# Optimization experiments

Measured on AMD Instinct MI355X. Metric: run time of the kernel, lower is better.

Reference implementation:

```python
import jax, jax.numpy as jnp
import numpy as np

N = 100000
E = 1600000
F_IN = 1024
H = 128
OUT = 32
EPS = 1e-07
TOTAL_COUNT = 10000.0
BN_EPS = 1e-5


def setup_inputs() -> dict:
    key = jax.random.key(0)
    ks = jax.random.split(key, 16)
    x = jax.random.uniform(ks[0], (N, F_IN), dtype=jnp.float32)
    edge_index = jax.random.randint(ks[1], (2, E), 0, N, dtype=jnp.int64)
    def nrm(k, shape, scale=0.05):
        return jax.random.normal(k, shape, dtype=jnp.float32) * scale
    return {
        "x": x,
        "edge_index": edge_index,
        "W0": nrm(ks[2], (F_IN, H)),
        "a_s0": nrm(ks[3], (H,)),
        "a_d0": nrm(ks[4], (H,)),
        "g0": jnp.ones((H,), jnp.float32),
        "b0": jnp.zeros((H,), jnp.float32),
        "W1": nrm(ks[5], (H, H)),
        "a_s1": nrm(ks[6], (H,)),
        "a_d1": nrm(ks[7], (H,)),
        "g1": jnp.ones((H,), jnp.float32),
        "b1": jnp.zeros((H,), jnp.float32),
        "locW": nrm(ks[8], (H, OUT)),
        "locb": jnp.zeros((OUT,), jnp.float32),
        "stdW": nrm(ks[9], (H, OUT)),
        "stdb": jnp.zeros((OUT,), jnp.float32),
    }


def gat_conv(h, src, dst, W, a_s, a_d, n_nodes):
    # PyG GATConv, heads=1, concat=False, no self-loops, no bias
    h2 = h @ W                       # [N, H]
    alpha_s = h2 @ a_s               # [N]
    alpha_d = h2 @ a_d               # [N]
    e = jax.nn.leaky_relu(alpha_s[src] + alpha_d[dst], 0.2)  # [E]
    m = jax.ops.segment_max(e, dst, num_segments=n_nodes)    # [N]
    w = jnp.exp(e - m[dst])                                  # [E]
    denom = jax.ops.segment_sum(w, dst, num_segments=n_nodes)
    msg = w[:, None] * h2[src]                               # [E, H]
    out = jax.ops.segment_sum(msg, dst, num_segments=n_nodes)
    return out / (denom[:, None] + 1e-16)


def batchnorm(h, gamma, beta):
    mu = jnp.mean(h, axis=0)
    var = jnp.mean(jnp.square(h - mu), axis=0)
    return gamma * (h - mu) * jax.lax.rsqrt(var + BN_EPS) + beta


def reference(x, edge_index, W0, a_s0, a_d0, g0, b0, W1, a_s1, a_d1, g1, b1,
              locW, locb, stdW, stdb):
    src, dst = edge_index[0], edge_index[1]
    n = x.shape[0]
    l = jnp.sum(x, axis=1, keepdims=True)                 # library size
    ptr = jnp.log1p(x * (TOTAL_COUNT / l))                # normalize
    for (W, a_s, a_d, g, b) in ((W0, a_s0, a_d0, g0, b0), (W1, a_s1, a_d1, g1, b1)):
        ptr = gat_conv(ptr, src, dst, W, a_s, a_d, n)
        ptr = batchnorm(ptr, g, b)
        ptr = jax.nn.leaky_relu(ptr, 0.2)
        # dropout = identity (eval mode)
    loc = ptr @ locW + locb
    std = jax.nn.softplus(ptr @ stdW + stdb) + EPS
    return (loc, std, l)
```

## Files before the change

### kernel.cpp

```cpp
#include <hip/hip_runtime.h>

#define NN 100000
#define EE 1600000
#define FIN 1024
#define HH 128
#define OUTD 32
#define TOTC 10000.0f

typedef float f32x4 __attribute__((ext_vector_type(4)));
typedef short bf16x8 __attribute__((ext_vector_type(8)));
typedef short short4v __attribute__((ext_vector_type(4)));

static __device__ __forceinline__ short f2bf(float f) {
    unsigned u = __float_as_uint(f);
    unsigned r = (u + 0x7fffu + ((u >> 16) & 1u)) >> 16;
    return (short)r;
}

__global__ void zero_k(int* __restrict__ p, int n) {
    int i = blockIdx.x * 256 + threadIdx.x;
    if (i < n) p[i] = 0;
}

__global__ __launch_bounds__(256) void rowsum_k(const float* __restrict__ x,
                                                float* __restrict__ lout) {
    int row = blockIdx.x;
    int tid = threadIdx.x;
    const float4* px = (const float4*)(x + (long)row * FIN);
    float4 v = px[tid];
    float s = v.x + v.y + v.z + v.w;
#pragma unroll
    for (int o = 32; o; o >>= 1) s += __shfl_xor(s, o);
    __shared__ float ws[4];
    if ((tid & 63) == 0) ws[tid >> 6] = s;
    __syncthreads();
    if (tid == 0) lout[row] = ws[0] + ws[1] + ws[2] + ws[3];
}

__global__ void convW0_k(const float* __restrict__ W, short* __restrict__ BT) {
    int idx = blockIdx.x * 256 + threadIdx.x;
    int n = idx >> 10, k = idx & 1023;
    BT[idx] = f2bf(W[(long)k * HH + n]);
}
__global__ void convW1_k(const float* __restrict__ W, short* __restrict__ BT) {
    int idx = blockIdx.x * 256 + threadIdx.x;
    int n = idx >> 7, k = idx & 127;
    BT[idx] = f2bf(W[k * HH + n]);
}
__global__ void convWH_k(const float* __restrict__ locW, const float* __restrict__ stdW,
                         short* __restrict__ BT) {
    int idx = blockIdx.x * 256 + threadIdx.x;
    int n = idx >> 7, k = idx & 127;
    float v = (n < 32) ? locW[k * OUTD + n] : ((n < 64) ? stdW[k * OUTD + (n - 32)] : 0.0f);
    BT[idx] = f2bf(v);
}

__global__ void hist_k(const int* __restrict__ dst, int* __restrict__ cnt, int e) {
    int i = blockIdx.x * 256 + threadIdx.x;
    if (i < e) atomicAdd(cnt + dst[i], 1);
}

__global__ __launch_bounds__(256) void scanA_k(const int* __restrict__ cnt,
                                               int* __restrict__ out,
                                               int* __restrict__ partials, int n) {
    __shared__ int sc[256];
    int tid = threadIdx.x;
    int base = blockIdx.x * 1024 + tid * 4;
    int c[4];
#pragma unroll
    for (int u = 0; u < 4; u++) c[u] = (base + u < n) ? cnt[base + u] : 0;
    int s = c[0] + c[1] + c[2] + c[3];
    sc[tid] = s;
    __syncthreads();
    for (int of = 1; of < 256; of <<= 1) {
        int v = (tid >= of) ? sc[tid - of] : 0;
        __syncthreads();
        sc[tid] += v;
        __syncthreads();
    }
    int e = sc[tid] - s;
#pragma unroll
    for (int u = 0; u < 4; u++) {
        if (base + u < n) out[base + u] = e;
        e += c[u];
    }
    if (tid == 255) partials[blockIdx.x] = sc[255];
}

__global__ __launch_bounds__(128) void scanB_k(int* __restrict__ partials, int nblk) {
    __shared__ int sc[128];
    int tid = threadIdx.x;
    int v = (tid < nblk) ? partials[tid] : 0;
    sc[tid] = v;
    __syncthreads();
    for (int of = 1; of < 128; of <<= 1) {
        int t2 = (tid >= of) ? sc[tid - of] : 0;
        __syncthreads();
        sc[tid] += t2;
        __syncthreads();
    }
    if (tid < nblk) partials[tid] = sc[tid] - v;
}

__global__ void scanC_k(int* __restrict__ rp, const int* __restrict__ offs, int n, int total) {
    int i = blockIdx.x * 256 + threadIdx.x;
    if (i < n) rp[i] += offs[i >> 10];
    if (i == 0) rp[n] = total;
}

__global__ void fill_k(const int* __restrict__ src, const int* __restrict__ dst,
                       const int* __restrict__ rp, int* __restrict__ cur,
                       int* __restrict__ cs, int e) {
    int i = blockIdx.x * 256 + threadIdx.x;
    if (i < e) {
        int d = dst[i];
        int p = atomicAdd(cur + d, 1);
        cs[rp[d] + p] = src[i];
    }
}

#define LDP 88

template <int ASRC, int EPI>
__global__ __launch_bounds__(256) void gemm_k(
    const void* __restrict__ Ap, const float* __restrict__ lvec,
    const short* __restrict__ BT, float* __restrict__ C,
    const float* __restrict__ bias_loc, const float* __restrict__ bias_std,
    float* __restrict__ out_loc, float* __restrict__ out_std, int M, int K) {
    __shared__ short sA[128 * LDP];
    __shared__ short sB[128 * LDP];
    __shared__ float sScale[128];
    const int tid = threadIdx.x;
    const int row0 = blockIdx.x * 128;
    if (ASRC == 0) {
        if (tid < 128) {
            int g = row0 + tid;
            sScale[tid] = (g < M) ? (TOTC / lvec[g]) : 0.0f;
        }
    }
    __syncthreads();

    const int lane = tid & 63;
    const int wv = tid >> 6;
    const int wm = (wv & 1) * 64, wn = (wv >> 1) * 64;
    const int lm = lane & 15, q = lane >> 4;

    f32x4 acc[4][4];
#pragma unroll
    for (int i = 0; i < 4; i++)
#pragma unroll
        for (int j = 0; j < 4; j++) acc[i][j] = {0.f, 0.f, 0.f, 0.f};

    const int r = tid >> 1;
    const int cb = (tid & 1) * 32;
    const int gr = row0 + r;

    for (int kk = 0; kk < K; kk += 64) {
        if (ASRC == 0) {
            const float* X = (const float*)Ap;
            const float s = sScale[r];
            if (gr < M) {
                const float4* px = (const float4*)(X + (long)gr * K + kk + cb);
#pragma unroll
                for (int u = 0; u < 8; ++u) {
                    float4 v = px[u];
                    short4v o;
                    o.x = f2bf(__logf(fmaf(v.x, s, 1.0f)));
                    o.y = f2bf(__logf(fmaf(v.y, s, 1.0f)));
                    o.z = f2bf(__logf(fmaf(v.z, s, 1.0f)));
                    o.w = f2bf(__logf(fmaf(v.w, s, 1.0f)));
                    *(short4v*)&sA[r * LDP + cb + u * 4] = o;
                }
            } else {
                short4v z;
                z.x = z.y = z.z = z.w = 0;
#pragma unroll
                for (int u = 0; u < 8; ++u) *(short4v*)&sA[r * LDP + cb + u * 4] = z;
            }
        } else {
            const short* A = (const short*)Ap;
            if (gr < M) {
                const short4v* pa = (const short4v*)(A + (long)gr * K + kk + cb);
#pragma unroll
                for (int u = 0; u < 8; ++u) *(short4v*)&sA[r * LDP + cb + u * 4] = pa[u];
            } else {
                short4v z;
                z.x = z.y = z.z = z.w = 0;
#pragma unroll
                for (int u = 0; u < 8; ++u) *(short4v*)&sA[r * LDP + cb + u * 4] = z;
            }
        }
        {
            const short4v* pb = (const short4v*)(BT + (long)r * K + kk + cb);
#pragma unroll
            for (int u = 0; u < 8; ++u) *(short4v*)&sB[r * LDP + cb + u * 4] = pb[u];
        }
        __syncthreads();
#pragma unroll
        for (int ks = 0; ks < 64; ks += 32) {
            bf16x8 af[4], bf[4];
#pragma unroll
            for (int i = 0; i < 4; i++)
                af[i] = *(const bf16x8*)&sA[(wm + i * 16 + lm) * LDP + ks + q * 8];
#pragma unroll
            for (int j = 0; j < 4; j++)
                bf[j] = *(const bf16x8*)&sB[(wn + j * 16 + lm) * LDP + ks + q * 8];
#pragma unroll
            for (int i = 0; i < 4; i++)
#pragma unroll
                for (int j = 0; j < 4; j++)
                    acc[i][j] = __builtin_amdgcn_mfma_f32_16x16x32_bf16(af[i], bf[j], acc[i][j], 0, 0, 0);
        }
        __syncthreads();
    }

    if (EPI == 0) {
#pragma unroll
        for (int i = 0; i < 4; i++)
#pragma unroll
            for (int rg = 0; rg < 4; rg++) {
                int grow = row0 + wm + i * 16 + q * 4 + rg;
                if (grow < M) {
#pragma unroll
                    for (int j = 0; j < 4; j++) {
                        int col = wn + j * 16 + lm;
                        C[(long)grow * HH + col] = acc[i][j][rg];
                    }
                }
            }
    } else {
        if (wn == 0) {
#pragma unroll
            for (int i = 0; i < 4; i++)
#pragma unroll
                for (int rg = 0; rg < 4; rg++) {
                    int grow = row0 + wm + i * 16 + q * 4 + rg;
                    if (grow < M) {
#pragma unroll
                        for (int j = 0; j < 4; j++) {
                            int col = j * 16 + lm;
                            float v = acc[i][j][rg];
                            if (col < 32) {
                                out_loc[(long)grow * OUTD + col] = v + bias_loc[col];
                            } else {
                                float xv = v + bias_std[col - 32];
                                float sp = fmaxf(xv, 0.f) + __logf(1.f + __expf(-fabsf(xv)));
                                out_std[(long)grow * OUTD + (col - 32)] = sp + 1e-7f;
                            }
                        }
                    }
                }
        }
    }
}

__global__ __launch_bounds__(256) void alpha_k(const float* __restrict__ h2,
                                               const float* __restrict__ avs,
                                               const float* __restrict__ avd,
                                               float* __restrict__ outs,
                                               float* __restrict__ outd, int n) {
    int lane = threadIdx.x & 63;
    int row = blockIdx.x * 4 + (threadIdx.x >> 6);
    if (row >= n) return;
    float2 v = *(const float2*)(h2 + (long)row * HH + 2 * lane);
    float ps = v.x * avs[2 * lane] + v.y * avs[2 * lane + 1];
    float pd = v.x * avd[2 * lane] + v.y * avd[2 * lane + 1];
#pragma unroll
    for (int o = 32; o; o >>= 1) {
        ps += __shfl_xor(ps, o);
        pd += __shfl_xor(pd, o);
    }
    if (lane == 0) {
        outs[row] = ps;
        outd[row] = pd;
    }
}

__global__ __launch_bounds__(256) void agg_k(const float* __restrict__ h2,
                                             const float* __restrict__ as,
                                             const float* __restrict__ ad,
                                             const int* __restrict__ row_ptr,
                                             const int* __restrict__ col_src,
                                             float* __restrict__ out, int n) {
    int lane = threadIdx.x & 63;
    int node = blockIdx.x * 4 + (threadIdx.x >> 6);
    if (node >= n) return;
    int s0 = row_ptr[node], s1 = row_ptr[node + 1];
    float adv = ad[node];
    float m = -INFINITY;
    for (int b = s0; b < s1; b += 64) {
        int idx = b + lane;
        if (idx < s1) {
            float e = as[col_src[idx]] + adv;
            e = (e > 0.f) ? e : 0.2f * e;
            m = fmaxf(m, e);
        }
    }
#pragma unroll
    for (int o = 32; o; o >>= 1) m = fmaxf(m, __shfl_xor(m, o));

    float acc0 = 0.f, acc1 = 0.f, wsum = 0.f;
    for (int b = s0; b < s1; b += 64) {
        int idx = b + lane;
        int cl = min(64, s1 - b);
        float w = 0.f;
        int s = 0;
        if (idx < s1) {
            s = col_src[idx];
            float e = as[s] + adv;
            e = (e > 0.f) ? e : 0.2f * e;
            w = __expf(e - m);
            wsum += w;
        }
        for (int j = 0; j < cl; ++j) {
            float wj = __shfl(w, j);
            int sj = __shfl(s, j);
            float2 hv = *(const float2*)(h2 + (long)sj * HH + 2 * lane);
            acc0 = fmaf(wj, hv.x, acc0);
            acc1 = fmaf(wj, hv.y, acc1);
        }
    }
#pragma unroll
    for (int o = 32; o; o >>= 1) wsum += __shfl_xor(wsum, o);
    float inv = 1.f / (wsum + 1e-16f);
    float2 o2;
    o2.x = acc0 * inv;
    o2.y = acc1 * inv;
    *(float2*)(out + (long)node * HH + 2 * lane) = o2;
}

__global__ __launch_bounds__(256) void bnstats_k(const float* __restrict__ h,
                                                 float* __restrict__ bsum,
                                                 float* __restrict__ bsq, int n) {
    int col = threadIdx.x & 127;
    int half = threadIdx.x >> 7;
    int stride = gridDim.x * 2;
    float s = 0.f, sq = 0.f;
    for (int row = blockIdx.x * 2 + half; row < n; row += stride) {
        float v = h[(long)row * HH + col];
        s += v;
        sq += v * v;
    }
    atomicAdd(bsum + col, s);
    atomicAdd(bsq + col, sq);
}

__global__ __launch_bounds__(256) void bnapply_k(const float* __restrict__ h,
                                                 const float* __restrict__ bsum,
                                                 const float* __restrict__ bsq,
                                                 const float* __restrict__ g,
                                                 const float* __restrict__ b,
                                                 short* __restrict__ obf, int n) {
    long idx = (long)blockIdx.x * 256 + threadIdx.x;
    long total = (long)n * 32;
    if (idx >= total) return;
    int col0 = ((int)(idx & 31)) * 4;
    float4 v = *(const float4*)(h + idx * 4);
    const float invn = 1.0f / (float)n;
    short4v o;
    float vv[4] = {v.x, v.y, v.z, v.w};
    short oo[4];
#pragma unroll
    for (int j = 0; j < 4; j++) {
        int c = col0 + j;
        float mu = bsum[c] * invn;
        float var = bsq[c] * invn - mu * mu;
        float rs = rsqrtf(var + 1e-5f);
        float val = (vv[j] - mu) * rs * g[c] + b[c];
        val = (val > 0.f) ? val : 0.2f * val;
        oo[j] = f2bf(val);
    }
    o.x = oo[0]; o.y = oo[1]; o.z = oo[2]; o.w = oo[3];
    *(short4v*)(obf + idx * 4) = o;
}

extern "C" void kernel_launch(void* const* d_in, const int* in_sizes, int n_in,
                              void* d_out, int out_size, void* d_ws, size_t ws_size,
                              hipStream_t stream) {
    const float* x = (const float*)d_in[0];
    const int* ei = (const int*)d_in[1];
    const int* srcp = ei;
    const int* dstp = ei + EE;
    const float* W0 = (const float*)d_in[2];
    const float* as0 = (const float*)d_in[3];
    const float* ad0 = (const float*)d_in[4];
    const float* g0 = (const float*)d_in[5];
    const float* b0 = (const float*)d_in[6];
    const float* W1 = (const float*)d_in[7];
    const float* as1 = (const float*)d_in[8];
    const float* ad1 = (const float*)d_in[9];
    const float* g1 = (const float*)d_in[10];
    const float* b1 = (const float*)d_in[11];
    const float* locW = (const float*)d_in[12];
    const float* locb = (const float*)d_in[13];
    const float* stdW = (const float*)d_in[14];
    const float* stdb = (const float*)d_in[15];

    float* out = (float*)d_out;
    float* out_loc = out;
    float* out_std = out + (long)NN * OUTD;
    float* lvec = out + 2L * NN * OUTD;

    char* wsb = (char*)d_ws;
    size_t off = 0;
    auto alloc = [&](size_t bytes) {
        size_t cur = off;
        off += (bytes + 255) & ~(size_t)255;
        return cur;
    };
    float* h2 = (float*)(wsb + alloc((size_t)NN * HH * 4));
    float* h_agg = (float*)(wsb + alloc((size_t)NN * HH * 4));
    short* ptrbf = (short*)(wsb + alloc((size_t)NN * HH * 2));
    int* col_src = (int*)(wsb + alloc((size_t)EE * 4));
    int* zreg = (int*)(wsb + alloc((size_t)(2 * NN + 256) * 4));
    int* counts = zreg;
    int* cursor = zreg + NN;
    float* bn_sum = (float*)(zreg + 2 * NN);
    float* bn_sq = bn_sum + 128;
    int* row_ptr = (int*)(wsb + alloc((size_t)(NN + 1) * 4));
    float* alpha_s = (float*)(wsb + alloc((size_t)NN * 4));
    float* alpha_d = (float*)(wsb + alloc((size_t)NN * 4));
    short* W0T = (short*)(wsb + alloc((size_t)HH * FIN * 2));
    short* W1T = (short*)(wsb + alloc((size_t)HH * HH * 2));
    short* WHT = (short*)(wsb + alloc((size_t)HH * HH * 2));
    int* partials = (int*)(wsb + alloc(512));

    const int ZN = 2 * NN + 256;
    zero_k<<<(ZN + 255) / 256, 256, 0, stream>>>(zreg, ZN);
    convW0_k<<<(HH * FIN) / 256, 256, 0, stream>>>(W0, W0T);
    convW1_k<<<(HH * HH) / 256, 256, 0, stream>>>(W1, W1T);
    convWH_k<<<(HH * HH) / 256, 256, 0, stream>>>(locW, stdW, WHT);
    rowsum_k<<<NN, 256, 0, stream>>>(x, lvec);

    hist_k<<<(EE + 255) / 256, 256, 0, stream>>>(dstp, counts, EE);
    scanA_k<<<(NN + 1023) / 1024, 256, 0, stream>>>(counts, row_ptr, partials, NN);
    scanB_k<<<1, 128, 0, stream>>>(partials, (NN + 1023) / 1024);
    scanC_k<<<(NN + 255) / 256, 256, 0, stream>>>(row_ptr, partials, NN, EE);
    fill_k<<<(EE + 255) / 256, 256, 0, stream>>>(srcp, dstp, row_ptr, cursor, col_src, EE);

    const int GB = (NN + 127) / 128;
    gemm_k<0, 0><<<GB, 256, 0, stream>>>(x, lvec, W0T, h2, nullptr, nullptr, nullptr, nullptr, NN, FIN);
    alpha_k<<<(NN + 3) / 4, 256, 0, stream>>>(h2, as0, ad0, alpha_s, alpha_d, NN);
    agg_k<<<(NN + 3) / 4, 256, 0, stream>>>(h2, alpha_s, alpha_d, row_ptr, col_src, h_agg, NN);
    bnstats_k<<<256, 256, 0, stream>>>(h_agg, bn_sum, bn_sq, NN);
    bnapply_k<<<(NN * 32 + 255) / 256, 256, 0, stream>>>(h_agg, bn_sum, bn_sq, g0, b0, ptrbf, NN);
    zero_k<<<1, 256, 0, stream>>>((int*)bn_sum, 256);
    gemm_k<1, 0><<<GB, 256, 0, stream>>>(ptrbf, nullptr, W1T, h2, nullptr, nullptr, nullptr, nullptr, NN, HH);
    alpha_k<<<(NN + 3) / 4, 256, 0, stream>>>(h2, as1, ad1, alpha_s, alpha_d, NN);
    agg_k<<<(NN + 3) / 4, 256, 0, stream>>>(h2, alpha_s, alpha_d, row_ptr, col_src, h_agg, NN);
    bnstats_k<<<256, 256, 0, stream>>>(h_agg, bn_sum, bn_sq, NN);
    bnapply_k<<<(NN * 32 + 255) / 256, 256, 0, stream>>>(h_agg, bn_sum, bn_sq, g1, b1, ptrbf, NN);
    gemm_k<1, 1><<<GB, 256, 0, stream>>>(ptrbf, nullptr, WHT, nullptr, locb, stdb, out_loc, out_std, NN, HH);
}
```

Before: 1.333 ms.

## Store GAT projections in bf16 and gather 4 edges per wave in aggregation

The GEMM epilogue now writes the projected features h2 as bf16 instead of fp32, and the alpha and aggregation kernels read that bf16 buffer. The aggregation kernel is restructured so each wave handles four edges at once, with 16 lanes each loading 8 bf16 features (16 bytes) per edge. The partial sums are then reduced across the lane groups with shuffles. This halves the gather traffic in the memory-bound edge aggregation and raises per-load width, at the cost of reduced precision in the messages and attention logits.

```diff
diff --git a/kernel.cpp b/kernel.cpp
--- a/kernel.cpp
+++ b/kernel.cpp
@@ -15,6 +15,9 @@
     unsigned u = __float_as_uint(f);
     unsigned r = (u + 0x7fffu + ((u >> 16) & 1u)) >> 16;
     return (short)r;
+}
+static __device__ __forceinline__ float bf2f(short s) {
+    return __uint_as_float(((unsigned)(unsigned short)s) << 16);
 }
 
 __global__ void zero_k(int* __restrict__ p, int n) {
@@ -124,7 +127,7 @@
 template <int ASRC, int EPI>
 __global__ __launch_bounds__(256) void gemm_k(
     const void* __restrict__ Ap, const float* __restrict__ lvec,
-    const short* __restrict__ BT, float* __restrict__ C,
+    const short* __restrict__ BT, short* __restrict__ Cbf,
     const float* __restrict__ bias_loc, const float* __restrict__ bias_std,
     float* __restrict__ out_loc, float* __restrict__ out_std, int M, int K) {
     __shared__ short sA[128 * LDP];
@@ -224,7 +227,7 @@
 #pragma unroll
                     for (int j = 0; j < 4; j++) {
                         int col = wn + j * 16 + lm;
-                        C[(long)grow * HH + col] = acc[i][j][rg];
+                        Cbf[(long)grow * HH + col] = f2bf(acc[i][j][rg]);
                     }
                 }
             }
@@ -254,7 +257,7 @@
     }
 }
 
-__global__ __launch_bounds__(256) void alpha_k(const float* __restrict__ h2,
+__global__ __launch_bounds__(256) void alpha_k(const short* __restrict__ h2bf,
                                                const float* __restrict__ avs,
                                                const float* __restrict__ avd,
                                                float* __restrict__ outs,
@@ -262,9 +265,11 @@
     int lane = threadIdx.x & 63;
     int row = blockIdx.x * 4 + (threadIdx.x >> 6);
     if (row >= n) return;
-    float2 v = *(const float2*)(h2 + (long)row * HH + 2 * lane);
-    float ps = v.x * avs[2 * lane] + v.y * avs[2 * lane + 1];
-    float pd = v.x * avd[2 * lane] + v.y * avd[2 * lane + 1];
+    unsigned pv = *(const unsigned*)(h2bf + (long)row * HH + 2 * lane);
+    float v0 = __uint_as_float((pv & 0xffffu) << 16);
+    float v1 = __uint_as_float(pv & 0xffff0000u);
+    float ps = v0 * avs[2 * lane] + v1 * avs[2 * lane + 1];
+    float pd = v0 * avd[2 * lane] + v1 * avd[2 * lane + 1];
 #pragma unroll
     for (int o = 32; o; o >>= 1) {
         ps += __shfl_xor(ps, o);
@@ -276,7 +281,7 @@
     }
 }
 
-__global__ __launch_bounds__(256) void agg_k(const float* __restrict__ h2,
+__global__ __launch_bounds__(256) void agg_k(const short* __restrict__ h2bf,
                                              const float* __restrict__ as,
                                              const float* __restrict__ ad,
                                              const int* __restrict__ row_ptr,
@@ -299,10 +304,15 @@
 #pragma unroll
     for (int o = 32; o; o >>= 1) m = fmaxf(m, __shfl_xor(m, o));
 
-    float acc0 = 0.f, acc1 = 0.f, wsum = 0.f;
+    const int eg = lane >> 4;
+    const int f8 = (lane & 15) * 8;
+    float accf[8];
+#pragma unroll
+    for (int u = 0; u < 8; u++) accf[u] = 0.f;
+    float wsum = 0.f;
+
     for (int b = s0; b < s1; b += 64) {
         int idx = b + lane;
-        int cl = min(64, s1 - b);
         float w = 0.f;
         int s = 0;
         if (idx < s1) {
@@ -312,21 +322,30 @@
             w = __expf(e - m);
             wsum += w;
         }
-        for (int j = 0; j < cl; ++j) {
+        int cl = min(64, s1 - b);
+        for (int j = eg; j < cl; j += 4) {
             float wj = __shfl(w, j);
             int sj = __shfl(s, j);
-            float2 hv = *(const float2*)(h2 + (long)sj * HH + 2 * lane);
-            acc0 = fmaf(wj, hv.x, acc0);
-            acc1 = fmaf(wj, hv.y, acc1);
+            bf16x8 hv = *(const bf16x8*)(h2bf + (long)sj * HH + f8);
+#pragma unroll
+            for (int u = 0; u < 8; u++)
+                accf[u] = fmaf(wj, bf2f(hv[u]), accf[u]);
         }
     }
 #pragma unroll
     for (int o = 32; o; o >>= 1) wsum += __shfl_xor(wsum, o);
+#pragma unroll
+    for (int u = 0; u < 8; u++) {
+        accf[u] += __shfl_xor(accf[u], 16);
+        accf[u] += __shfl_xor(accf[u], 32);
+    }
     float inv = 1.f / (wsum + 1e-16f);
-    float2 o2;
-    o2.x = acc0 * inv;
-    o2.y = acc1 * inv;
-    *(float2*)(out + (long)node * HH + 2 * lane) = o2;
+    if (eg == 0) {
+        f32x4 o1 = {accf[0] * inv, accf[1] * inv, accf[2] * inv, accf[3] * inv};
+        f32x4 o2 = {accf[4] * inv, accf[5] * inv, accf[6] * inv, accf[7] * inv};
+        *(f32x4*)(out + (long)node * HH + f8) = o1;
+        *(f32x4*)(out + (long)node * HH + f8 + 4) = o2;
+    }
 }
 
 __global__ __launch_bounds__(256) void bnstats_k(const float* __restrict__ h,
@@ -408,7 +427,7 @@
         off += (bytes + 255) & ~(size_t)255;
         return cur;
     };
-    float* h2 = (float*)(wsb + alloc((size_t)NN * HH * 4));
+    short* h2bf = (short*)(wsb + alloc((size_t)NN * HH * 2));
     float* h_agg = (float*)(wsb + alloc((size_t)NN * HH * 4));
     short* ptrbf = (short*)(wsb + alloc((size_t)NN * HH * 2));
     int* col_src = (int*)(wsb + alloc((size_t)EE * 4));
@@ -439,15 +458,15 @@
     fill_k<<<(EE + 255) / 256, 256, 0, stream>>>(srcp, dstp, row_ptr, cursor, col_src, EE);
 
     const int GB = (NN + 127) / 128;
-    gemm_k<0, 0><<<GB, 256, 0, stream>>>(x, lvec, W0T, h2, nullptr, nullptr, nullptr, nullptr, NN, FIN);
-    alpha_k<<<(NN + 3) / 4, 256, 0, stream>>>(h2, as0, ad0, alpha_s, alpha_d, NN);
-    agg_k<<<(NN + 3) / 4, 256, 0, stream>>>(h2, alpha_s, alpha_d, row_ptr, col_src, h_agg, NN);
+    gemm_k<0, 0><<<GB, 256, 0, stream>>>(x, lvec, W0T, h2bf, nullptr, nullptr, nullptr, nullptr, NN, FIN);
+    alpha_k<<<(NN + 3) / 4, 256, 0, stream>>>(h2bf, as0, ad0, alpha_s, alpha_d, NN);
+    agg_k<<<(NN + 3) / 4, 256, 0, stream>>>(h2bf, alpha_s, alpha_d, row_ptr, col_src, h_agg, NN);
     bnstats_k<<<256, 256, 0, stream>>>(h_agg, bn_sum, bn_sq, NN);
     bnapply_k<<<(NN * 32 + 255) / 256, 256, 0, stream>>>(h_agg, bn_sum, bn_sq, g0, b0, ptrbf, NN);
     zero_k<<<1, 256, 0, stream>>>((int*)bn_sum, 256);
-    gemm_k<1, 0><<<GB, 256, 0, stream>>>(ptrbf, nullptr, W1T, h2, nullptr, nullptr, nullptr, nullptr, NN, HH);
-    alpha_k<<<(NN + 3) / 4, 256, 0, stream>>>(h2, as1, ad1, alpha_s, alpha_d, NN);
-    agg_k<<<(NN + 3) / 4, 256, 0, stream>>>(h2, alpha_s, alpha_d, row_ptr, col_src, h_agg, NN);
+    gemm_k<1, 0><<<GB, 256, 0, stream>>>(ptrbf, nullptr, W1T, h2bf, nullptr, nullptr, nullptr, nullptr, NN, HH);
+    alpha_k<<<(NN + 3) / 4, 256, 0, stream>>>(h2bf, as1, ad1, alpha_s, alpha_d, NN);
+    agg_k<<<(NN + 3) / 4, 256, 0, stream>>>(h2bf, alpha_s, alpha_d, row_ptr, col_src, h_agg, NN);
     bnstats_k<<<256, 256, 0, stream>>>(h_agg, bn_sum, bn_sq, NN);
     bnapply_k<<<(NN * 32 + 255) / 256, 256, 0, stream>>>(h_agg, bn_sum, bn_sq, g1, b1, ptrbf, NN);
     gemm_k<1, 1><<<GB, 256, 0, stream>>>(ptrbf, nullptr, WHT, nullptr, locb, stdb, out_loc, out_std, NN, HH);
```

Measured after the change: 1.206 ms. 9.5% less time.
